# Optimization experiments

Measured on AMD Instinct MI355X. Metric: run time of the kernel, lower is better.

The kernel has to match this reference:

```python
import jax, jax.numpy as jnp
import numpy as np

D_MODEL = 2048
D_STATE = 128
D_CONV = 4
EXPAND = 2
HEADDIM = 64
CHUNK = 64
D_INNER = EXPAND * D_MODEL            # 4096
NHEADS = D_INNER // HEADDIM           # 64
CONV_DIM = D_INNER + 2 * D_STATE      # 4352
D_IN_PROJ = 2 * D_INNER + 2 * D_STATE + NHEADS  # 8512
BATCH, SEQLEN = 2, 2048


def segsum(x):
    """Stable segment sum. x: (..., T) -> (..., T, T)."""
    T = x.shape[-1]
    xx = jnp.broadcast_to(x[..., :, None], x.shape + (T,))  # [.., d, e] = x[.., d]
    mask_lower = jnp.tril(jnp.ones((T, T), dtype=bool), -1)
    s = jnp.cumsum(jnp.where(mask_lower, xx, 0.0), axis=-2)
    mask_diag = jnp.tril(jnp.ones((T, T), dtype=bool), 0)
    return jnp.where(mask_diag, s, -jnp.inf)


def ssd(x, A, Bm, Cm, chunk):
    """x: [b,L,h,p], A: [b,L,h], Bm/Cm: [b,L,n]."""
    b, L, h, p = x.shape
    c = L // chunk
    x = x.reshape(b, c, chunk, h, p)
    A = A.reshape(b, c, chunk, h).transpose(0, 3, 1, 2)     # b h c l
    Bm = Bm.reshape(b, c, chunk, -1)                         # b c l n
    Cm = Cm.reshape(b, c, chunk, -1)
    A_cum = jnp.cumsum(A, axis=-1)                           # b h c l
    Lmat = jnp.exp(segsum(A))                                # b h c l s
    # intra-chunk (diagonal) output
    Y_diag = jnp.einsum('bcln,bcsn,bhcls,bcshp->bclhp', Cm, Bm, Lmat, x)
    # per-chunk states
    decay_states = jnp.exp(A_cum[..., -1:] - A_cum)          # b h c l
    states = jnp.einsum('bcln,bhcl,bclhp->bchpn', Bm, decay_states, x)
    init = jnp.zeros_like(states[:, :1])
    states = jnp.concatenate([init, states], axis=1)         # b (c+1) h p n
    # inter-chunk recurrence via segsum over chunk-level decays
    A_last = jnp.pad(A_cum[..., -1], ((0, 0), (0, 0), (1, 0)))  # b h (c+1)
    decay_chunk = jnp.exp(segsum(A_last))                    # b h (c+1) (c+1)
    new_states = jnp.einsum('bhzc,bchpn->bzhpn', decay_chunk, states)
    states, final_state = new_states[:, :-1], new_states[:, -1]
    # state -> output
    out_decay = jnp.exp(A_cum)                               # b h c l
    Y_off = jnp.einsum('bcln,bchpn,bhcl->bclhp', Cm, states, out_decay)
    return (Y_diag + Y_off).reshape(b, L, h, p), final_state


def setup_inputs() -> dict:
    key = jax.random.key(0)
    ks = jax.random.split(key, 8)
    u = jax.random.normal(ks[0], (BATCH, SEQLEN, D_MODEL), jnp.float32)
    W_in = jax.random.normal(ks[1], (D_MODEL, D_IN_PROJ), jnp.float32) / np.sqrt(D_MODEL).astype(np.float32)
    conv_w = jax.random.normal(ks[2], (CONV_DIM, D_CONV), jnp.float32) * np.sqrt(2.0 / D_CONV).astype(np.float32)
    conv_b = jnp.zeros((CONV_DIM,), jnp.float32)
    dt_bias = jax.random.uniform(ks[3], (NHEADS,), jnp.float32, minval=-2.0, maxval=2.0)
    A_log = jax.random.normal(ks[4], (NHEADS,), jnp.float32) * 0.1
    D_param = jnp.ones((NHEADS,), jnp.float32)
    norm_w = jnp.ones((D_INNER,), jnp.float32)
    W_out = jax.random.normal(ks[5], (D_INNER, D_MODEL), jnp.float32) / np.sqrt(D_INNER).astype(np.float32)
    return {'u': u, 'W_in': W_in, 'conv_w': conv_w, 'conv_b': conv_b,
            'dt_bias': dt_bias, 'A_log': A_log, 'D_param': D_param,
            'norm_w': norm_w, 'W_out': W_out}


def reference(u, W_in, conv_w, conv_b, dt_bias, A_log, D_param, norm_w, W_out):
    b, L, _ = u.shape
    zxbcdt = u @ W_in                                        # [b, L, 2*din + 2*n + h]
    z = zxbcdt[..., :D_INNER]
    xBC = zxbcdt[..., D_INNER:D_INNER + CONV_DIM]
    dt = zxbcdt[..., D_INNER + CONV_DIM:]
    dt = jax.nn.softplus(dt + dt_bias)                       # [b, L, h]
    # causal depthwise conv1d (kernel D_CONV, groups=channels)
    xp = jnp.pad(xBC, ((0, 0), (D_CONV - 1, 0), (0, 0)))
    xBC = sum(xp[:, w:w + L, :] * conv_w[:, w] for w in range(D_CONV)) + conv_b
    xBC = jax.nn.silu(xBC)
    x = xBC[..., :D_INNER]
    Bm = xBC[..., D_INNER:D_INNER + D_STATE]                 # [b, L, n]
    Cm = xBC[..., D_INNER + D_STATE:]                        # [b, L, n]
    x = x.reshape(b, L, NHEADS, HEADDIM)
    A = -jnp.exp(A_log)                                      # [h]
    y, final_state = ssd(x * dt[..., None], A * dt, Bm, Cm, CHUNK)
    y = y + x * D_param[:, None]                             # skip term
    y = y.reshape(b, L, D_INNER)
    # gated RMSNorm (fp32)
    yf = y * jax.nn.silu(z)
    rrms = jax.lax.rsqrt(jnp.mean(yf * yf, axis=-1, keepdims=True) + 1e-5)
    y = yf * rrms * norm_w
    return y @ W_out
```

## Files before the change

### kernel.cpp

```cpp
#include <hip/hip_runtime.h>

typedef unsigned short u16;
typedef __attribute__((ext_vector_type(8))) short bhalf8;
typedef __attribute__((ext_vector_type(4))) float floatx4;

__device__ __forceinline__ u16 f2bf(float f) {
    union { float f; unsigned u; } v; v.f = f;
    unsigned u = v.u;
    unsigned r = u + 0x7fffu + ((u >> 16) & 1u);
    return (u16)(r >> 16);
}
__device__ __forceinline__ float b2f(u16 h) {
    union { unsigned u; float f; } v; v.u = ((unsigned)h) << 16; return v.f;
}
__device__ __forceinline__ void unpack2(unsigned u, float& lo, float& hi) {
    union { unsigned u; float f; } a, b;
    a.u = u << 16; b.u = u & 0xffff0000u;
    lo = a.f; hi = b.f;
}
__device__ __forceinline__ void load_lds16(const void* g, void* l) {
    __builtin_amdgcn_global_load_lds(
        (const __attribute__((address_space(1))) unsigned int*)g,
        (__attribute__((address_space(3))) unsigned int*)l, 16, 0, 0);
}

__global__ void k_f2b4(const float* __restrict__ in, u16* __restrict__ out, int n4) {
    int i = blockIdx.x * 256 + threadIdx.x;
    if (i < n4) {
        float4 v = ((const float4*)in)[i];
        unsigned lo = (unsigned)f2bf(v.x) | ((unsigned)f2bf(v.y) << 16);
        unsigned hi = (unsigned)f2bf(v.z) | ((unsigned)f2bf(v.w) << 16);
        ((uint2*)out)[i] = make_uint2(lo, hi);
    }
}

__global__ void k_transpose_f2b(const float* __restrict__ W, u16* __restrict__ Wt,
                                int K, int N) {
    __shared__ float tile[32][33];
    int nt = blockIdx.x * 32, kt = blockIdx.y * 32;
    int tx = threadIdx.x, ty = threadIdx.y;
    #pragma unroll
    for (int r = 0; r < 32; r += 8) {
        int k = kt + ty + r, n = nt + tx;
        tile[ty + r][tx] = (n < N && k < K) ? W[(size_t)k * N + n] : 0.f;
    }
    __syncthreads();
    #pragma unroll
    for (int r = 0; r < 32; r += 8) {
        int n = nt + ty + r, k = kt + tx;
        Wt[(size_t)n * K + k] = f2bf(tile[tx][ty + r]);
    }
}

template <int EPI>
__global__ __launch_bounds__(256) void gemm_bt(
    const u16* __restrict__ A, const u16* __restrict__ Bt, int M, int N, int K,
    float* __restrict__ outF,
    u16* __restrict__ zb, u16* __restrict__ xbc, float* __restrict__ dtq,
    const float* __restrict__ dt_bias) {
    __shared__ u16 As[2 * 8192];
    __shared__ u16 Bs[2 * 8192];
    int t = threadIdx.x;
    int w = t >> 6, lane = t & 63;
    int m0 = blockIdx.y * 128, n0 = blockIdx.x * 128;
    int wm = (w >> 1) * 64, wn = (w & 1) * 64;
    floatx4 acc[4][4];
    #pragma unroll
    for (int i = 0; i < 4; i++)
        #pragma unroll
        for (int j = 0; j < 4; j++) acc[i][j] = (floatx4){0.f, 0.f, 0.f, 0.f};

    const int nt = K >> 6;
    const int byte0 = (w * 4) * 1024 + lane * 16;

    auto stage = [&](int sel, int k0) {
        #pragma unroll
        for (int i = 0; i < 4; i++) {
            int byte = byte0 + i * 1024;
            int row = byte >> 7;
            int colb = (byte & 127) ^ ((row & 7) << 4);
            load_lds16(A + (size_t)(m0 + row) * K + k0 + (colb >> 1),
                       (char*)As + sel * 16384 + byte);
            load_lds16(Bt + (size_t)(n0 + row) * K + k0 + (colb >> 1),
                       (char*)Bs + sel * 16384 + byte);
        }
    };

    stage(0, 0);
    __syncthreads();
    int cur = 0;
    for (int kt = 0; kt < nt; ++kt) {
        if (kt + 1 < nt) stage(cur ^ 1, (kt + 1) << 6);
        const u16* Ab = As + cur * 8192;
        const u16* Bb = Bs + cur * 8192;
        #pragma unroll
        for (int ks = 0; ks < 2; ks++) {
            int kk = ks * 32 + ((lane >> 4) << 3);
            bhalf8 af[4], bf[4];
            #pragma unroll
            for (int mi = 0; mi < 4; mi++) {
                int row = wm + mi * 16 + (lane & 15);
                int idx = (row * 64 + kk) ^ ((row & 7) << 3);
                af[mi] = *(const bhalf8*)(Ab + idx);
            }
            #pragma unroll
            for (int ni = 0; ni < 4; ni++) {
                int col = wn + ni * 16 + (lane & 15);
                int idx = (col * 64 + kk) ^ ((col & 7) << 3);
                bf[ni] = *(const bhalf8*)(Bb + idx);
            }
            #pragma unroll
            for (int mi = 0; mi < 4; mi++)
                #pragma unroll
                for (int ni = 0; ni < 4; ni++)
                    acc[mi][ni] = __builtin_amdgcn_mfma_f32_16x16x32_bf16(
                        af[mi], bf[ni], acc[mi][ni], 0, 0, 0);
        }
        __syncthreads();
        cur ^= 1;
    }
    #pragma unroll
    for (int mi = 0; mi < 4; mi++) {
        #pragma unroll
        for (int ni = 0; ni < 4; ni++) {
            floatx4 v = acc[mi][ni];
            int col = n0 + wn + ni * 16 + (lane & 15);
            #pragma unroll
            for (int r = 0; r < 4; r++) {
                int row = m0 + wm + mi * 16 + ((lane >> 4) << 2) + r;
                float val = v[r];
                if (EPI == 0) {
                    outF[(size_t)row * N + col] = val;
                } else {
                    if (col < 4096) {
                        zb[(size_t)row * 4096 + col] = f2bf(val);
                    } else if (col < 8448) {
                        xbc[(size_t)row * 4352 + (col - 4096)] = f2bf(val);
                    } else if (col < 8512) {
                        int h = col - 8448;
                        float xv = val + dt_bias[h];
                        float sp = (xv > 20.f) ? xv : log1pf(__expf(xv));
                        dtq[(size_t)row * 64 + h] = sp;
                    }
                }
            }
        }
    }
}

__global__ __launch_bounds__(256) void k_conv(
    const u16* __restrict__ xbc, const float* __restrict__ conv_w,
    const float* __restrict__ conv_b,
    u16* __restrict__ x, u16* __restrict__ Bo, u16* __restrict__ Co) {
    int bid = blockIdx.x;
    int b = bid >> 8, lt = bid & 255;
    int l0 = lt * 8;
    size_t rb = (size_t)(b * 2048) * 4352;
    for (int ch = threadIdx.x; ch < 4352; ch += 256) {
        float w0 = conv_w[ch * 4 + 0], w1 = conv_w[ch * 4 + 1];
        float w2 = conv_w[ch * 4 + 2], w3 = conv_w[ch * 4 + 3];
        float bc = conv_b[ch];
        float h0 = (l0 >= 3) ? b2f(xbc[rb + (size_t)(l0 - 3) * 4352 + ch]) : 0.f;
        float h1 = (l0 >= 2) ? b2f(xbc[rb + (size_t)(l0 - 2) * 4352 + ch]) : 0.f;
        float h2 = (l0 >= 1) ? b2f(xbc[rb + (size_t)(l0 - 1) * 4352 + ch]) : 0.f;
        #pragma unroll
        for (int i = 0; i < 8; i++) {
            int l = l0 + i;
            float xc = b2f(xbc[rb + (size_t)l * 4352 + ch]);
            float acc = bc + w0 * h0 + w1 * h1 + w2 * h2 + w3 * xc;
            float v = acc / (1.f + __expf(-acc));
            int row = b * 2048 + l;
            if (ch < 4096) {
                x[(size_t)row * 4096 + ch] = f2bf(v);
            } else if (ch < 4224) {
                Bo[(size_t)row * 128 + (ch - 4096)] = f2bf(v);
            } else {
                Co[(size_t)row * 128 + (ch - 4224)] = f2bf(v);
            }
            h0 = h1; h1 = h2; h2 = xc;
        }
    }
}

__global__ void k_dtprep(const float* __restrict__ dtq, const float* __restrict__ A_log,
                         float* __restrict__ acum, float* __restrict__ Tc) {
    int bc = blockIdx.x;
    int h = threadIdx.x;
    float A = -__expf(A_log[h]);
    float s = 0.f;
    #pragma unroll
    for (int l = 0; l < 64; l++) {
        int row = bc * 64 + l;
        s += A * dtq[row * 64 + h];
        acum[(size_t)row * 64 + h] = s;
    }
    int b = bc >> 5, c = bc & 31;
    Tc[(b * 64 + h) * 32 + c] = s;
}

__global__ __launch_bounds__(256) void k_G(const u16* __restrict__ Bo, const u16* __restrict__ Co,
                                           float* __restrict__ G) {
    int bc = blockIdx.x;
    int lq = blockIdx.y;
    __shared__ float BsT[128][68];
    __shared__ float Cs[16][132];
    int t = threadIdx.x;
    for (int idx = t; idx < 64 * 128; idx += 256) {
        int r = idx >> 7, n = idx & 127;
        BsT[n][r] = b2f(Bo[(size_t)(bc * 64 + r) * 128 + n]);
    }
    for (int idx = t; idx < 16 * 128; idx += 256) {
        int r = idx >> 7, n = idx & 127;
        Cs[r][n] = b2f(Co[(size_t)(bc * 64 + lq * 16 + r) * 128 + n]);
    }
    __syncthreads();
    int lr = t >> 4, sq = t & 15;
    int l = lq * 16 + lr;
    float a[4] = {0.f, 0.f, 0.f, 0.f};
    for (int n = 0; n < 128; n++) {
        float cv = Cs[lr][n];
        const float4* bp = (const float4*)&BsT[n][sq * 4];
        float4 b0 = bp[0];
        a[0] += cv * b0.x; a[1] += cv * b0.y; a[2] += cv * b0.z; a[3] += cv * b0.w;
    }
    size_t gb = ((size_t)bc * 64 + l) * 64 + sq * 4;
    #pragma unroll
    for (int i = 0; i < 4; i++) G[gb + i] = a[i];
}

__global__ __launch_bounds__(256) void k_diag(
    const u16* __restrict__ xb, const u16* __restrict__ Bo,
    const float* __restrict__ G, const float* __restrict__ acum,
    const float* __restrict__ dtq,
    u16* __restrict__ y, u16* __restrict__ cs) {
    int bc = blockIdx.x, h = blockIdx.y;
    __shared__ u16 XT[4096];
    __shared__ u16 Pl[4096];
    __shared__ u16 BTd[8192];
    __shared__ float ac[64], dec[64], dts[64];
    int t = threadIdx.x, w = t >> 6, lane = t & 63;
    if (t < 64) {
        ac[t] = acum[(size_t)(bc * 64 + t) * 64 + h];
        dts[t] = dtq[(size_t)(bc * 64 + t) * 64 + h];
    }
    __syncthreads();
    if (t < 64) dec[t] = __expf(ac[63] - ac[t]);
    for (int idx = t; idx < 4096; idx += 256) {
        int s = idx >> 6, p = idx & 63;
        float v = b2f(xb[(size_t)(bc * 64 + s) * 4096 + h * 64 + p]) * dts[s];
        XT[(p << 6) + (s ^ ((p & 7) << 3))] = f2bf(v);
    }
    for (int idx = t; idx < 4096; idx += 256) {
        int l = idx >> 6, s = idx & 63;
        float v = (s <= l) ? __expf(ac[l] - ac[s]) * G[((size_t)bc * 64 + l) * 64 + s] : 0.f;
        Pl[(l << 6) + (s ^ ((l & 7) << 3))] = f2bf(v);
    }
    __syncthreads();
    for (int idx = t; idx < 8192; idx += 256) {
        int l = idx >> 7, n = idx & 127;
        float v = b2f(Bo[(size_t)(bc * 64 + l) * 128 + n]) * dec[l];
        BTd[(n << 6) + (l ^ ((n & 7) << 3))] = f2bf(v);
    }
    __syncthreads();
    {
        floatx4 accY[4];
        #pragma unroll
        for (int ni = 0; ni < 4; ni++) accY[ni] = (floatx4){0.f, 0.f, 0.f, 0.f};
        int row = (w << 4) + (lane & 15);
        #pragma unroll
        for (int ks = 0; ks < 2; ks++) {
            int k = (ks << 5) + ((lane >> 4) << 3);
            int kx = k ^ ((row & 7) << 3);
            bhalf8 af = *(const bhalf8*)(Pl + (row << 6) + kx);
            #pragma unroll
            for (int ni = 0; ni < 4; ni++) {
                int pr = (ni << 4) + (lane & 15);
                bhalf8 bf = *(const bhalf8*)(XT + (pr << 6) + kx);
                accY[ni] = __builtin_amdgcn_mfma_f32_16x16x32_bf16(af, bf, accY[ni], 0, 0, 0);
            }
        }
        #pragma unroll
        for (int ni = 0; ni < 4; ni++) {
            int col = (ni << 4) + (lane & 15);
            #pragma unroll
            for (int r = 0; r < 4; r++) {
                int l = (w << 4) + ((lane >> 4) << 2) + r;
                y[(size_t)(bc * 64 + l) * 4096 + h * 64 + col] = f2bf(accY[ni][r]);
            }
        }
    }
    {
        floatx4 accS[8];
        #pragma unroll
        for (int ni = 0; ni < 8; ni++) accS[ni] = (floatx4){0.f, 0.f, 0.f, 0.f};
        int prow = (w << 4) + (lane & 15);
        #pragma unroll
        for (int ks = 0; ks < 2; ks++) {
            int k = (ks << 5) + ((lane >> 4) << 3);
            int kx = k ^ ((prow & 7) << 3);
            bhalf8 af = *(const bhalf8*)(XT + (prow << 6) + kx);
            #pragma unroll
            for (int ni = 0; ni < 8; ni++) {
                int nr = (ni << 4) + (lane & 15);
                bhalf8 bf = *(const bhalf8*)(BTd + (nr << 6) + kx);
                accS[ni] = __builtin_amdgcn_mfma_f32_16x16x32_bf16(af, bf, accS[ni], 0, 0, 0);
            }
        }
        #pragma unroll
        for (int ni = 0; ni < 8; ni++) {
            int n = (ni << 4) + (lane & 15);
            #pragma unroll
            for (int r = 0; r < 4; r++) {
                int p = (w << 4) + ((lane >> 4) << 2) + r;
                cs[((size_t)(bc * 64 + h) * 64 + p) * 128 + n] = f2bf(accS[ni][r]);
            }
        }
    }
}

__global__ __launch_bounds__(256) void k_scan(u16* __restrict__ cs, const float* __restrict__ Tc) {
    int bid = blockIdx.x;
    int bh = bid >> 5, pb = bid & 31;
    int b = bh >> 6, h = bh & 63;
    int pn = pb * 256 + threadIdx.x;
    const float* Tp = Tc + bh * 32;
    size_t stride = (size_t)64 * 8192;
    size_t base = (((size_t)(b * 32) * 64) + h) * 8192 + pn;
    float v[32];
    #pragma unroll
    for (int c = 0; c < 32; c++) v[c] = b2f(cs[base + (size_t)c * stride]);
    float P = 0.f;
    #pragma unroll
    for (int c = 0; c < 32; c++) {
        float tmp = v[c];
        cs[base + (size_t)c * stride] = f2bf(P);
        P = __expf(Tp[c]) * P + tmp;
    }
}

__global__ __launch_bounds__(256) void k_yoff(
    const u16* __restrict__ Co, const u16* __restrict__ cs,
    const float* __restrict__ acum, u16* __restrict__ y) {
    int bc = blockIdx.x, h = blockIdx.y;
    __shared__ u16 Cl[8192];
    __shared__ u16 Sl[8192];
    __shared__ float od[64];
    int t = threadIdx.x, w = t >> 6, lane = t & 63;
    for (int idx = t; idx < 8192; idx += 256) {
        int l = idx >> 7, n = idx & 127;
        Cl[(l << 7) + (n ^ ((l & 15) << 3))] = Co[(size_t)(bc * 64 + l) * 128 + n];
    }
    size_t pbase = ((size_t)bc * 64 + h) * 8192;
    for (int idx = t; idx < 8192; idx += 256) {
        int p = idx >> 7, n = idx & 127;
        Sl[(p << 7) + (n ^ ((p & 15) << 3))] = cs[pbase + idx];
    }
    if (t < 64) od[t] = __expf(acum[(size_t)(bc * 64 + t) * 64 + h]);
    __syncthreads();
    floatx4 acc[4];
    #pragma unroll
    for (int ni = 0; ni < 4; ni++) acc[ni] = (floatx4){0.f, 0.f, 0.f, 0.f};
    int lrow = (w << 4) + (lane & 15);
    #pragma unroll
    for (int ks = 0; ks < 4; ks++) {
        int k = (ks << 5) + ((lane >> 4) << 3);
        int kx = k ^ ((lrow & 15) << 3);
        bhalf8 af = *(const bhalf8*)(Cl + (lrow << 7) + kx);
        #pragma unroll
        for (int ni = 0; ni < 4; ni++) {
            int pr = (ni << 4) + (lane & 15);
            bhalf8 bf = *(const bhalf8*)(Sl + (pr << 7) + kx);
            acc[ni] = __builtin_amdgcn_mfma_f32_16x16x32_bf16(af, bf, acc[ni], 0, 0, 0);
        }
    }
    #pragma unroll
    for (int ni = 0; ni < 4; ni++) {
        int col = (ni << 4) + (lane & 15);
        #pragma unroll
        for (int r = 0; r < 4; r++) {
            int l = (w << 4) + ((lane >> 4) << 2) + r;
            size_t yi = (size_t)(bc * 64 + l) * 4096 + h * 64 + col;
            y[yi] = f2bf(b2f(y[yi]) + od[l] * acc[ni][r]);
        }
    }
}

__global__ __launch_bounds__(256) void k_norm(
    const u16* __restrict__ y, const u16* __restrict__ x, const u16* __restrict__ z,
    const float* __restrict__ D_param, const float* __restrict__ norm_w,
    u16* __restrict__ ynorm) {
    int row = blockIdx.x;
    int t = threadIdx.x;
    size_t base = (size_t)row * 4096 + (size_t)t * 16;
    float yv[16], xf[16], zf[16];
    {
        uint4 a = ((const uint4*)(y + base))[0];
        uint4 b = ((const uint4*)(y + base))[1];
        unpack2(a.x, yv[0], yv[1]); unpack2(a.y, yv[2], yv[3]);
        unpack2(a.z, yv[4], yv[5]); unpack2(a.w, yv[6], yv[7]);
        unpack2(b.x, yv[8], yv[9]); unpack2(b.y, yv[10], yv[11]);
        unpack2(b.z, yv[12], yv[13]); unpack2(b.w, yv[14], yv[15]);
    }
    {
        uint4 a = ((const uint4*)(x + base))[0];
        uint4 b = ((const uint4*)(x + base))[1];
        unpack2(a.x, xf[0], xf[1]); unpack2(a.y, xf[2], xf[3]);
        unpack2(a.z, xf[4], xf[5]); unpack2(a.w, xf[6], xf[7]);
        unpack2(b.x, xf[8], xf[9]); unpack2(b.y, xf[10], xf[11]);
        unpack2(b.z, xf[12], xf[13]); unpack2(b.w, xf[14], xf[15]);
    }
    {
        uint4 a = ((const uint4*)(z + base))[0];
        uint4 b = ((const uint4*)(z + base))[1];
        unpack2(a.x, zf[0], zf[1]); unpack2(a.y, zf[2], zf[3]);
        unpack2(a.z, zf[4], zf[5]); unpack2(a.w, zf[6], zf[7]);
        unpack2(b.x, zf[8], zf[9]); unpack2(b.y, zf[10], zf[11]);
        unpack2(b.z, zf[12], zf[13]); unpack2(b.w, zf[14], zf[15]);
    }
    float D = D_param[t >> 2];
    float vals[16], ss = 0.f;
    #pragma unroll
    for (int j = 0; j < 16; j++) {
        float v = yv[j] + xf[j] * D;
        float zz = zf[j];
        float yf = v * (zz / (1.f + __expf(-zz)));
        vals[j] = yf;
        ss += yf * yf;
    }
    #pragma unroll
    for (int o = 32; o > 0; o >>= 1) ss += __shfl_down(ss, o, 64);
    __shared__ float red[4];
    if ((t & 63) == 0) red[t >> 6] = ss;
    __syncthreads();
    float tot = red[0] + red[1] + red[2] + red[3];
    float rr = rsqrtf(tot * (1.f / 4096.f) + 1e-5f);
    unsigned o32[8];
    #pragma unroll
    for (int j = 0; j < 8; j++) {
        float lo = vals[2 * j] * rr * norm_w[t * 16 + 2 * j];
        float hi = vals[2 * j + 1] * rr * norm_w[t * 16 + 2 * j + 1];
        o32[j] = (unsigned)f2bf(lo) | ((unsigned)f2bf(hi) << 16);
    }
    uint4 w0, w1;
    w0.x = o32[0]; w0.y = o32[1]; w0.z = o32[2]; w0.w = o32[3];
    w1.x = o32[4]; w1.y = o32[5]; w1.z = o32[6]; w1.w = o32[7];
    ((uint4*)(ynorm + base))[0] = w0;
    ((uint4*)(ynorm + base))[1] = w1;
}

extern "C" void kernel_launch(void* const* d_in, const int* in_sizes, int n_in,
                              void* d_out, int out_size, void* d_ws, size_t ws_size,
                              hipStream_t stream) {
    const float* u       = (const float*)d_in[0];
    const float* W_in    = (const float*)d_in[1];
    const float* conv_w  = (const float*)d_in[2];
    const float* conv_b  = (const float*)d_in[3];
    const float* dt_bias = (const float*)d_in[4];
    const float* A_log   = (const float*)d_in[5];
    const float* D_param = (const float*)d_in[6];
    const float* norm_w  = (const float*)d_in[7];
    const float* W_out   = (const float*)d_in[8];
    float* out = (float*)d_out;

    const size_t REGION = (size_t)134217728;
    size_t need = REGION
                + (size_t)33554432
                + (size_t)33554432
                + (size_t)1048576
                + (size_t)1048576
                + (size_t)1048576
                + (size_t)16384
                + (size_t)1048576
                + (size_t)1048576
                + (size_t)33554432;
    if (ws_size < need) return;

    char* ws = (char*)d_ws;
    u16*   ubf   = (u16*)(ws);
    u16*   WinT  = (u16*)(ws + 16777216);
    u16*   xbc   = (u16*)(ws + 16777216 + 35651584);
    u16*   cs    = (u16*)(ws);
    u16*   WoutT = (u16*)(ws);
    u16*   ynorm = (u16*)(ws + 16777216);
    char* p = ws + REGION;
    u16*   zb    = (u16*)p;            p += 33554432;
    u16*   xb    = (u16*)p;            p += 33554432;
    u16*   Bo    = (u16*)p;            p += 1048576;
    u16*   Co    = (u16*)p;            p += 1048576;
    float* acum  = (float*)p;          p += 1048576;
    float* Tc    = (float*)p;          p += 16384;
    float* G     = (float*)p;          p += 1048576;
    float* dtq   = (float*)p;          p += 1048576;
    u16*   yb    = (u16*)p;            p += 33554432;

    k_f2b4<<<8192, 256, 0, stream>>>(u, ubf, 4096 * 2048 / 4);
    k_transpose_f2b<<<dim3(268, 64), dim3(32, 8), 0, stream>>>(W_in, WinT, 2048, 8512);
    gemm_bt<1><<<dim3(67, 32), 256, 0, stream>>>(ubf, WinT, 4096, 8576, 2048,
                                                 nullptr, zb, xbc, dtq, dt_bias);
    k_conv<<<512, 256, 0, stream>>>(xbc, conv_w, conv_b, xb, Bo, Co);
    k_dtprep<<<64, 64, 0, stream>>>(dtq, A_log, acum, Tc);
    k_G<<<dim3(64, 4), 256, 0, stream>>>(Bo, Co, G);
    k_diag<<<dim3(64, 64), 256, 0, stream>>>(xb, Bo, G, acum, dtq, yb, cs);
    k_scan<<<4096, 256, 0, stream>>>(cs, Tc);
    k_yoff<<<dim3(64, 64), 256, 0, stream>>>(Co, cs, acum, yb);
    k_transpose_f2b<<<dim3(64, 128), dim3(32, 8), 0, stream>>>(W_out, WoutT, 4096, 2048);
    k_norm<<<4096, 256, 0, stream>>>(yb, xb, zb, D_param, norm_w, ynorm);
    gemm_bt<0><<<dim3(16, 32), 256, 0, stream>>>(ynorm, WoutT, 4096, 2048, 4096,
                                                 out, nullptr, nullptr, nullptr, nullptr);
    (void)in_sizes; (void)n_in; (void)out_size;
}
```

Measured before the change: 607.0 us.

## Fuse inter-chunk state scan with off-diagonal output into one per-head kernel

Result: slower. 673.1 us (+10.9%).

```diff
diff --git a/kernel.cpp b/kernel.cpp
--- a/kernel.cpp
+++ b/kernel.cpp
@@ -318,70 +318,67 @@
     }
 }
 
-__global__ __launch_bounds__(256) void k_scan(u16* __restrict__ cs, const float* __restrict__ Tc) {
-    int bid = blockIdx.x;
-    int bh = bid >> 5, pb = bid & 31;
+__global__ __launch_bounds__(512) void k_scanyoff(
+    const u16* __restrict__ Co, const u16* __restrict__ cs,
+    const float* __restrict__ acum, const float* __restrict__ Tc,
+    u16* __restrict__ y) {
+    int bh = blockIdx.x;
     int b = bh >> 6, h = bh & 63;
-    int pn = pb * 256 + threadIdx.x;
-    const float* Tp = Tc + bh * 32;
-    size_t stride = (size_t)64 * 8192;
-    size_t base = (((size_t)(b * 32) * 64) + h) * 8192 + pn;
-    float v[32];
-    #pragma unroll
-    for (int c = 0; c < 32; c++) v[c] = b2f(cs[base + (size_t)c * stride]);
-    float P = 0.f;
-    #pragma unroll
-    for (int c = 0; c < 32; c++) {
-        float tmp = v[c];
-        cs[base + (size_t)c * stride] = f2bf(P);
-        P = __expf(Tp[c]) * P + tmp;
-    }
-}
-
-__global__ __launch_bounds__(256) void k_yoff(
-    const u16* __restrict__ Co, const u16* __restrict__ cs,
-    const float* __restrict__ acum, u16* __restrict__ y) {
-    int bc = blockIdx.x, h = blockIdx.y;
     __shared__ u16 Cl[8192];
-    __shared__ u16 Sl[8192];
+    __shared__ u16 Pbf[8192];
+    __shared__ u16 Sc[8192];
+    __shared__ float P32[8192];
     __shared__ float od[64];
     int t = threadIdx.x, w = t >> 6, lane = t & 63;
-    for (int idx = t; idx < 8192; idx += 256) {
-        int l = idx >> 7, n = idx & 127;
-        Cl[(l << 7) + (n ^ ((l & 15) << 3))] = Co[(size_t)(bc * 64 + l) * 128 + n];
-    }
-    size_t pbase = ((size_t)bc * 64 + h) * 8192;
-    for (int idx = t; idx < 8192; idx += 256) {
-        int p = idx >> 7, n = idx & 127;
-        Sl[(p << 7) + (n ^ ((p & 15) << 3))] = cs[pbase + idx];
-    }
-    if (t < 64) od[t] = __expf(acum[(size_t)(bc * 64 + t) * 64 + h]);
-    __syncthreads();
-    floatx4 acc[4];
-    #pragma unroll
-    for (int ni = 0; ni < 4; ni++) acc[ni] = (floatx4){0.f, 0.f, 0.f, 0.f};
-    int lrow = (w << 4) + (lane & 15);
-    #pragma unroll
-    for (int ks = 0; ks < 4; ks++) {
-        int k = (ks << 5) + ((lane >> 4) << 3);
-        int kx = k ^ ((lrow & 15) << 3);
-        bhalf8 af = *(const bhalf8*)(Cl + (lrow << 7) + kx);
-        #pragma unroll
-        for (int ni = 0; ni < 4; ni++) {
-            int pr = (ni << 4) + (lane & 15);
-            bhalf8 bf = *(const bhalf8*)(Sl + (pr << 7) + kx);
-            acc[ni] = __builtin_amdgcn_mfma_f32_16x16x32_bf16(af, bf, acc[ni], 0, 0, 0);
-        }
-    }
-    #pragma unroll
-    for (int ni = 0; ni < 4; ni++) {
-        int col = (ni << 4) + (lane & 15);
-        #pragma unroll
-        for (int r = 0; r < 4; r++) {
-            int l = (w << 4) + ((lane >> 4) << 2) + r;
-            size_t yi = (size_t)(bc * 64 + l) * 4096 + h * 64 + col;
-            y[yi] = f2bf(b2f(y[yi]) + od[l] * acc[ni][r]);
-        }
+    for (int i = t; i < 8192; i += 512) P32[i] = 0.f;
+    const float* Tp = Tc + bh * 32;
+    const int lt = w >> 1, ph = w & 1;
+    int lrow = (lt << 4) + (lane & 15);
+    for (int c = 0; c < 32; ++c) {
+        int bc = b * 32 + c;
+        for (int idx = t; idx < 8192; idx += 512) {
+            int l = idx >> 7, n = idx & 127;
+            Cl[(l << 7) + (n ^ ((l & 15) << 3))] = Co[(size_t)(bc * 64 + l) * 128 + n];
+            Sc[idx] = cs[(size_t)(bc * 64 + h) * 8192 + idx];
+        }
+        if (t < 64) od[t] = __expf(acum[(size_t)(bc * 64 + t) * 64 + h]);
+        __syncthreads();
+        if (c > 0) {
+            floatx4 acc[2];
+            acc[0] = (floatx4){0.f, 0.f, 0.f, 0.f};
+            acc[1] = (floatx4){0.f, 0.f, 0.f, 0.f};
+            #pragma unroll
+            for (int ks = 0; ks < 4; ks++) {
+                int k = (ks << 5) + ((lane >> 4) << 3);
+                int kx = k ^ ((lrow & 15) << 3);
+                bhalf8 af = *(const bhalf8*)(Cl + (lrow << 7) + kx);
+                #pragma unroll
+                for (int j = 0; j < 2; j++) {
+                    int pr = ((ph * 2 + j) << 4) + (lane & 15);
+                    bhalf8 bf = *(const bhalf8*)(Pbf + (pr << 7) + kx);
+                    acc[j] = __builtin_amdgcn_mfma_f32_16x16x32_bf16(af, bf, acc[j], 0, 0, 0);
+                }
+            }
+            #pragma unroll
+            for (int j = 0; j < 2; j++) {
+                int col = ((ph * 2 + j) << 4) + (lane & 15);
+                #pragma unroll
+                for (int r = 0; r < 4; r++) {
+                    int l = (lt << 4) + ((lane >> 4) << 2) + r;
+                    size_t yi = (size_t)(bc * 64 + l) * 4096 + h * 64 + col;
+                    y[yi] = f2bf(b2f(y[yi]) + od[l] * acc[j][r]);
+                }
+            }
+        }
+        __syncthreads();
+        float eT = __expf(Tp[c]);
+        for (int idx = t; idx < 8192; idx += 512) {
+            float pv = eT * P32[idx] + b2f(Sc[idx]);
+            P32[idx] = pv;
+            int p = idx >> 7, n = idx & 127;
+            Pbf[(p << 7) + (n ^ ((p & 15) << 3))] = f2bf(pv);
+        }
+        __syncthreads();
     }
 }
 
@@ -501,8 +498,7 @@
     k_dtprep<<<64, 64, 0, stream>>>(dtq, A_log, acum, Tc);
     k_G<<<dim3(64, 4), 256, 0, stream>>>(Bo, Co, G);
     k_diag<<<dim3(64, 64), 256, 0, stream>>>(xb, Bo, G, acum, dtq, yb, cs);
-    k_scan<<<4096, 256, 0, stream>>>(cs, Tc);
-    k_yoff<<<dim3(64, 64), 256, 0, stream>>>(Co, cs, acum, yb);
+    k_scanyoff<<<128, 512, 0, stream>>>(Co, cs, acum, Tc, yb);
     k_transpose_f2b<<<dim3(64, 128), dim3(32, 8), 0, stream>>>(W_out, WoutT, 4096, 2048);
     k_norm<<<4096, 256, 0, stream>>>(yb, xb, zb, D_param, norm_w, ynorm);
     gemm_bt<0><<<dim3(16, 32), 256, 0, stream>>>(ynorm, WoutT, 4096, 2048, 4096,
```
